# Optimization experiments

Measured on AMD Instinct MI355X. Metric: run time of the kernel, lower is better.

## Reference

```python
import jax, jax.numpy as jnp
import numpy as np
from jax import lax

B, T, C = 512, 128, 66
H, L, W = 512, 2, 10


def gru_cell(x, h, W_ih, W_hh, b_ih, b_hh):
    # PyTorch GRU gate order: r, z, n
    gi = x @ W_ih.T + b_ih            # [B, 3H]
    gh = h @ W_hh.T + b_hh            # [B, 3H]
    i_r, i_z, i_n = jnp.split(gi, 3, axis=-1)
    h_r, h_z, h_n = jnp.split(gh, 3, axis=-1)
    r = jax.nn.sigmoid(i_r + h_r)
    z = jax.nn.sigmoid(i_z + h_z)
    n = jnp.tanh(i_n + r * h_n)
    return (1.0 - z) * n + z * h


def setup_inputs() -> dict:
    key = jax.random.key(0)
    ks = jax.random.split(key, 16)
    s = 0.02
    inp = {
        "x": jax.random.normal(ks[0], (B, T, C), jnp.float32),
        # GRU layer 0 (input C -> hidden H)
        "W_ih0": jax.random.normal(ks[1], (3 * H, C), jnp.float32) * s,
        "W_hh0": jax.random.normal(ks[2], (3 * H, H), jnp.float32) * s,
        "b_ih0": jnp.zeros((3 * H,), jnp.float32),
        "b_hh0": jnp.zeros((3 * H,), jnp.float32),
        # GRU layer 1 (hidden H -> hidden H)
        "W_ih1": jax.random.normal(ks[3], (3 * H, H), jnp.float32) * s,
        "W_hh1": jax.random.normal(ks[4], (3 * H, H), jnp.float32) * s,
        "b_ih1": jnp.zeros((3 * H,), jnp.float32),
        "b_hh1": jnp.zeros((3 * H,), jnp.float32),
        # temporal_fc: Linear(window_size, 1) -> weight [1, W], bias [1]
        "temporal_w": jax.random.normal(ks[5], (1, W), jnp.float32) * s,
        "temporal_b": jnp.zeros((1,), jnp.float32),
        # spatial_fc: Linear(H, C)
        "spatial_w": jax.random.normal(ks[6], (C, H), jnp.float32) * s,
        "spatial_b": jnp.zeros((C,), jnp.float32),
    }
    return inp


def _forward(x, W_ih0, W_hh0, b_ih0, b_hh0, W_ih1, W_hh1, b_ih1, b_hh1,
             temporal_w, temporal_b, spatial_w, spatial_b):
    p0 = (W_ih0, W_hh0, b_ih0, b_hh0)
    p1 = (W_ih1, W_hh1, b_ih1, b_hh1)

    # ---- encoder: 2-layer GRU over the full sequence ----
    xs = jnp.transpose(x, (1, 0, 2))  # [T, B, C]
    h0 = jnp.zeros((x.shape[0], H), x.dtype)

    def make_step(p):
        def step(h, xt):
            hn = gru_cell(xt, h, *p)
            return hn, hn
        return step

    hT0, ys0 = lax.scan(make_step(p0), h0, xs)          # ys0 [T,B,H]
    hT1, ys1 = lax.scan(make_step(p1), h0, ys0)         # ys1 [T,B,H]

    encoder_window = jnp.transpose(ys1[-W:], (1, 0, 2))  # [B, W, H]
    last_input_frame = x[:, -1, :]                       # [B, C]

    def dec_step(carry, _):
        (h_0, h_1), win, dec_in = carry
        h_0n = gru_cell(dec_in, h_0, *p0)
        h_1n = gru_cell(h_0n, h_1, *p1)                  # decoder_out [B,H]
        win = jnp.concatenate([win[:, 1:, :], h_1n[:, None, :]], axis=1)
        # temporal_fc over window axis: [B,W,H] -> [B,H]
        t = jnp.einsum('bwh,w->bh', win, temporal_w[0]) + temporal_b[0]
        frame = t @ spatial_w.T + spatial_b + dec_in     # recursive residual
        return ((h_0n, h_1n), win, frame), frame

    init = ((hT0, hT1), encoder_window, last_input_frame)
    _, frames = lax.scan(dec_step, init, None, length=T)  # [T,B,C]
    return jnp.transpose(frames, (1, 0, 2))               # [B,T,C]


def reference(x, W_ih0, W_hh0, b_ih0, b_hh0, W_ih1, W_hh1, b_ih1, b_hh1,
              temporal_w, temporal_b, spatial_w, spatial_b):
    return _forward(x, W_ih0, W_hh0, b_ih0, b_hh0, W_ih1, W_hh1, b_ih1, b_hh1,
                    temporal_w, temporal_b, spatial_w, spatial_b)
```

## Files before the change

### kernel.cpp

```cpp
#include <hip/hip_runtime.h>
#include <hip/hip_bf16.h>

typedef __attribute__((ext_vector_type(8))) short bf16x8;
typedef __attribute__((ext_vector_type(4))) float f32x4;

#define NB 512
#define NT 128
#define NC 66
#define NH 512
#define NW 10
#define CP 96
#define BM 32
#define BJ 64
#define BK 32
#define BKP 40
#define NWG 256
#define NTHR 256
#define G3 1536

struct Params {
  const float *x, *Wih0, *Whh0, *bih0, *bhh0, *Wih1, *Whh1, *bih1, *bhh1, *tw, *tb, *sw, *sb;
  float *out;
  unsigned *barL, *barG;
  __hip_bfloat16 *Wih0h, *Wih0l;
  __hip_bfloat16 *Wch, *Wcl;
  float *cb;
  float *h0, *h1, *tvec;
  __hip_bfloat16 *winb;
};

__device__ __forceinline__ float sigmoidf_(float x) { return 1.f / (1.f + __expf(-x)); }
__device__ __forceinline__ float tanhf_(float x) {
  float e = __expf(2.f * x);
  return (e - 1.f) / (e + 1.f);
}
__device__ __forceinline__ void split2(float v, __hip_bfloat16& h, __hip_bfloat16& l) {
  h = __float2bfloat16(v);
  l = __float2bfloat16(v - __bfloat162float(h));
}
__device__ __forceinline__ unsigned short bfbits(__hip_bfloat16 h) { return *(unsigned short*)&h; }
__device__ __forceinline__ void splitpack4(float4 v, ushort4& ph, ushort4& pl) {
  __hip_bfloat16 h, l;
  split2(v.x, h, l); ph.x = bfbits(h); pl.x = bfbits(l);
  split2(v.y, h, l); ph.y = bfbits(h); pl.y = bfbits(l);
  split2(v.z, h, l); ph.z = bfbits(h); pl.z = bfbits(l);
  split2(v.w, h, l); ph.w = bfbits(h); pl.w = bfbits(l);
}

__device__ __forceinline__ float4 cload4(const float* p) {
  unsigned long long a = __hip_atomic_load((const unsigned long long*)p,       __ATOMIC_RELAXED, __HIP_MEMORY_SCOPE_AGENT);
  unsigned long long b = __hip_atomic_load(((const unsigned long long*)p) + 1, __ATOMIC_RELAXED, __HIP_MEMORY_SCOPE_AGENT);
  float4 r;
  ((unsigned long long*)&r)[0] = a;
  ((unsigned long long*)&r)[1] = b;
  return r;
}

__device__ __forceinline__ void gbar(unsigned* barL, unsigned* barG, unsigned& phase,
                                     int tid, int grp) {
  __syncthreads();
  ++phase;
  if (tid == 0) {
    unsigned old = __hip_atomic_fetch_add(&barL[grp * 32], 1u, __ATOMIC_RELEASE,
                                          __HIP_MEMORY_SCOPE_AGENT);
    if (old == phase * 32 - 1)
      __hip_atomic_fetch_add(barG, 1u, __ATOMIC_RELAXED, __HIP_MEMORY_SCOPE_AGENT);
    while (__hip_atomic_load(barG, __ATOMIC_RELAXED, __HIP_MEMORY_SCOPE_AGENT) < phase)
      __builtin_amdgcn_s_sleep(2);
  }
  __syncthreads();
  asm volatile("" ::: "memory");
}

#define AM_X 0
#define AM_H 2

__device__ __forceinline__ float4 loadA(int amode, const float* __restrict__ A, int tstep,
                                        int b0, int am, int k) {
  if (amode == AM_X) {
    const float* xr = A + ((size_t)(b0 + am) * NT + tstep) * NC;
    float4 v;
    v.x = (k + 0 < NC) ? xr[k + 0] : 0.f;
    v.y = (k + 1 < NC) ? xr[k + 1] : 0.f;
    v.z = (k + 2 < NC) ? xr[k + 2] : 0.f;
    v.w = (k + 3 < NC) ? xr[k + 3] : 0.f;
    return v;
  }
  return cload4(A + (size_t)(b0 + am) * NH + k);
}

__device__ __forceinline__ void zacc(f32x4 acc[2][4]) {
#pragma unroll
  for (int i = 0; i < 2; ++i)
#pragma unroll
    for (int g = 0; g < 4; ++g) {
      acc[i][g][0] = 0.f; acc[i][g][1] = 0.f; acc[i][g][2] = 0.f; acc[i][g][3] = 0.f;
    }
}

template <int G2, bool PSW>
__device__ __forceinline__ void gemm_tile(
    f32x4 acc[2][4],
    const __hip_bfloat16* __restrict__ Wh, const __hip_bfloat16* __restrict__ Wl,
    const float* __restrict__ Wf, int Kb,
    int amode, const float* __restrict__ A, int tstep,
    int b0, int j0,
    __hip_bfloat16* AsH, __hip_bfloat16* AsL,
    __hip_bfloat16* BsH, __hip_bfloat16* BsL,
    int tid)
{
  const int wv = tid >> 6, lane = tid & 63, quad = lane >> 4, l15 = lane & 15;
  const int ms = wv & 1, jh = wv >> 1;
  const int am = tid >> 3;
  const int ak = (tid & 7) << 2;
  const int nk = Kb >> 5;

  uint4 bh_[3], bl_[3];
  float4 w0_[3], w1_[3];

  auto fetchB = [&](int st) {
    const int kb = st << 5;
#pragma unroll
    for (int r = 0; r < 3; ++r) {
      const int l = tid + r * NTHR;
      const int nl = l >> 2, k8 = (l & 3) << 3;
      const int g = nl >> 6, jl = nl & 63;
      if (PSW) {
        const size_t o = (size_t)(g * NH + j0 + jl) * Kb + kb + k8;
        bh_[r] = *(const uint4*)(Wh + o);
        bl_[r] = *(const uint4*)(Wl + o);
      } else {
        const float* wp = Wf + (size_t)(g * NH + j0 + jl) * Kb + kb + k8;
        w0_[r] = *(const float4*)wp;
        w1_[r] = *(const float4*)(wp + 4);
      }
    }
  };

  float4 av = loadA(amode, A, tstep, b0, am, ak);
  fetchB(0);

  for (int st = 0; st < nk; ++st) {
    const int cur = st & 1;
    __hip_bfloat16* ah_d = AsH + cur * (BM * BKP);
    __hip_bfloat16* al_d = AsL + cur * (BM * BKP);
    __hip_bfloat16* bh_d = BsH + cur * (3 * BJ * BKP);
    __hip_bfloat16* bl_d = BsL + cur * (3 * BJ * BKP);
    {
      ushort4 ph, pl;
      splitpack4(av, ph, pl);
      *(ushort4*)(ah_d + am * BKP + ak) = ph;
      *(ushort4*)(al_d + am * BKP + ak) = pl;
    }
#pragma unroll
    for (int r = 0; r < 3; ++r) {
      const int l = tid + r * NTHR;
      const int nl = l >> 2, k8 = (l & 3) << 3;
      if (PSW) {
        *(uint4*)(bh_d + nl * BKP + k8) = bh_[r];
        *(uint4*)(bl_d + nl * BKP + k8) = bl_[r];
      } else {
        ushort4 ph0, pl0, ph1, pl1;
        splitpack4(w0_[r], ph0, pl0);
        splitpack4(w1_[r], ph1, pl1);
        *(ushort4*)(bh_d + nl * BKP + k8) = ph0;
        *(ushort4*)(bh_d + nl * BKP + k8 + 4) = ph1;
        *(ushort4*)(bl_d + nl * BKP + k8) = pl0;
        *(ushort4*)(bl_d + nl * BKP + k8 + 4) = pl1;
      }
    }
    if (st + 1 < nk) {
      av = loadA(amode, A, tstep, b0, am, ((st + 1) << 5) + ak);
      fetchB(st + 1);
    }
    __syncthreads();
    bf16x8 ah = *(const bf16x8*)(ah_d + (ms * 16 + l15) * BKP + quad * 8);
    bf16x8 al = *(const bf16x8*)(al_d + (ms * 16 + l15) * BKP + quad * 8);
#pragma unroll
    for (int jlf = 0; jlf < 2; ++jlf) {
      const int nbase = (jh * 32 + jlf * 16 + l15) * BKP + quad * 8;
      {
        bf16x8 bh = *(const bf16x8*)(bh_d + nbase);
        bf16x8 bl = *(const bf16x8*)(bl_d + nbase);
        acc[jlf][0] = __builtin_amdgcn_mfma_f32_16x16x32_bf16(ah, bh, acc[jlf][0], 0, 0, 0);
        acc[jlf][0] = __builtin_amdgcn_mfma_f32_16x16x32_bf16(al, bh, acc[jlf][0], 0, 0, 0);
        acc[jlf][0] = __builtin_amdgcn_mfma_f32_16x16x32_bf16(ah, bl, acc[jlf][0], 0, 0, 0);
      }
      {
        bf16x8 bh = *(const bf16x8*)(bh_d + BJ * BKP + nbase);
        bf16x8 bl = *(const bf16x8*)(bl_d + BJ * BKP + nbase);
        acc[jlf][1] = __builtin_amdgcn_mfma_f32_16x16x32_bf16(ah, bh, acc[jlf][1], 0, 0, 0);
        acc[jlf][1] = __builtin_amdgcn_mfma_f32_16x16x32_bf16(al, bh, acc[jlf][1], 0, 0, 0);
        acc[jlf][1] = __builtin_amdgcn_mfma_f32_16x16x32_bf16(ah, bl, acc[jlf][1], 0, 0, 0);
      }
      {
        bf16x8 bh = *(const bf16x8*)(bh_d + 2 * BJ * BKP + nbase);
        bf16x8 bl = *(const bf16x8*)(bl_d + 2 * BJ * BKP + nbase);
        acc[jlf][G2] = __builtin_amdgcn_mfma_f32_16x16x32_bf16(ah, bh, acc[jlf][G2], 0, 0, 0);
        acc[jlf][G2] = __builtin_amdgcn_mfma_f32_16x16x32_bf16(al, bh, acc[jlf][G2], 0, 0, 0);
        acc[jlf][G2] = __builtin_amdgcn_mfma_f32_16x16x32_bf16(ah, bl, acc[jlf][G2], 0, 0, 0);
      }
    }
  }
  __syncthreads();
}

__device__ __forceinline__ void ew_gru(
    f32x4 acc[2][4],
    const float* __restrict__ bi, const float* __restrict__ bh,
    const float* __restrict__ hold, float* __restrict__ hnew,
    int b0, int j0, int tid, __hip_bfloat16* win, int slot)
{
  const int wv = tid >> 6, lane = tid & 63, quad = lane >> 4, l15 = lane & 15;
  const int ms = wv & 1, jh = wv >> 1;
#pragma unroll
  for (int jlf = 0; jlf < 2; ++jlf) {
    const int j = j0 + jh * 32 + jlf * 16 + l15;
    const float br = bi[j] + bh[j];
    const float bz = bi[NH + j] + bh[NH + j];
    const float bni = bi[2 * NH + j];
    const float bnh = bh[2 * NH + j];
#pragma unroll
    for (int rg = 0; rg < 4; ++rg) {
      const int b = b0 + ms * 16 + quad * 4 + rg;
      const float r = sigmoidf_(acc[jlf][0][rg] + br);
      const float z = sigmoidf_(acc[jlf][1][rg] + bz);
      const float n = tanhf_(acc[jlf][2][rg] + bni + r * (acc[jlf][3][rg] + bnh));
      const float h = hold[(size_t)b * NH + j];
      const float hn = (1.f - z) * n + z * h;
      hnew[(size_t)b * NH + j] = hn;
      if (win) win[((size_t)b * NW + slot) * NH + j] = __float2bfloat16(hn);
    }
  }
}

__device__ __forceinline__ void ew_dec1(
    f32x4 acc[2][4], const Params& P, float* __restrict__ h1p,
    int b0, int j0, int tid, int s)
{
  const int wv = tid >> 6, lane = tid & 63, quad = lane >> 4, l15 = lane & 15;
  const int ms = wv & 1, jh = wv >> 1;
  const int slot = s % NW;
  float twv[NW];
#pragma unroll
  for (int k = 0; k < NW; ++k) {
    int idx = k - slot - 1; if (idx < 0) idx += NW;
    twv[k] = P.tw[idx];
  }
  const float tw9 = P.tw[NW - 1];
  const float tb0 = P.tb[0];
#pragma unroll
  for (int jlf = 0; jlf < 2; ++jlf) {
    const int j = j0 + jh * 32 + jlf * 16 + l15;
    const float br = P.bih1[j] + P.bhh1[j];
    const float bz = P.bih1[NH + j] + P.bhh1[NH + j];
    const float bni = P.bih1[2 * NH + j];
    const float bnh = P.bhh1[2 * NH + j];
#pragma unroll
    for (int rg = 0; rg < 4; ++rg) {
      const int b = b0 + ms * 16 + quad * 4 + rg;
      const float r = sigmoidf_(acc[jlf][0][rg] + br);
      const float z = sigmoidf_(acc[jlf][1][rg] + bz);
      const float n = tanhf_(acc[jlf][2][rg] + bni + r * (acc[jlf][3][rg] + bnh));
      const float h = h1p[(size_t)b * NH + j];
      const float hn = (1.f - z) * n + z * h;
      h1p[(size_t)b * NH + j] = hn;
      __hip_bfloat16* wrow = P.winb + (size_t)b * NW * NH + j;
      wrow[(size_t)slot * NH] = __float2bfloat16(hn);
      float ts = tb0 + hn * tw9;
#pragma unroll
      for (int k = 0; k < NW; ++k) {
        if (k == slot) continue;
        ts += __bfloat162float(wrow[(size_t)k * NH]) * twv[k];
      }
      P.tvec[(size_t)b * NH + j] = ts;
    }
  }
}

__global__ __launch_bounds__(NTHR) void rnn_kernel(Params P) {
  __shared__ __align__(16) __hip_bfloat16 AsH[2 * BM * BKP];
  __shared__ __align__(16) __hip_bfloat16 AsL[2 * BM * BKP];
  __shared__ __align__(16) __hip_bfloat16 BsH[2 * 3 * BJ * BKP];
  __shared__ __align__(16) __hip_bfloat16 BsL[2 * 3 * BJ * BKP];
  __shared__ __align__(16) float tl[4 * NH];
  const int tid = threadIdx.x;
  const int wg = blockIdx.x;
  const int grp = wg & 7;
  const size_t gid = (size_t)wg * NTHR + tid;
  const size_t GT = (size_t)NWG * NTHR;
  unsigned phase = 0;
  const int wv = tid >> 6, lane = tid & 63, l15 = lane & 15;
  const int jh = wv >> 1;

  for (size_t i = gid; i < (size_t)G3 * CP; i += GT) {
    const int row = (int)(i / CP), k = (int)(i - (size_t)row * CP);
    split2(k < NC ? P.Wih0[(size_t)row * NC + k] : 0.f, P.Wih0h[i], P.Wih0l[i]);
  }
  for (size_t i = gid; i < (size_t)G3 * NH; i += GT) {
    const int r = (int)(i >> 9), h = (int)(i & (NH - 1));
    float a = 0.f;
    for (int c = 0; c < NC; ++c) a += P.Wih0[(size_t)r * NC + c] * P.sw[(size_t)c * NH + h];
    split2(a, P.Wch[i], P.Wcl[i]);
  }
  for (size_t i = gid; i < (size_t)G3; i += GT) {
    float a = 0.f;
    for (int c = 0; c < NC; ++c) a += P.Wih0[i * NC + c] * P.sb[c];
    P.cb[i] = a;
  }
  for (size_t i = gid; i < (size_t)2 * NB * NH; i += GT) { P.h0[i] = 0.f; P.h1[i] = 0.f; }
  gbar(P.barL, P.barG, phase, tid, grp);

  const bool isL1 = wg >= 128;
  const int tile = wg & 127;
  const int b0 = (tile >> 3) * BM;
  const int j0 = (tile & 7) * BJ;

  float G[2][3][4];

  for (int t = 0; t <= NT; ++t) {
    const int cur = t & 1;
    float* h0c = P.h0 + (size_t)cur * NB * NH;
    float* h0n = P.h0 + (size_t)(cur ^ 1) * NB * NH;
    float* h1c = P.h1 + (size_t)cur * NB * NH;
    float* h1n = P.h1 + (size_t)(cur ^ 1) * NB * NH;
    f32x4 acc[2][4];
    if (!isL1) {
      if (t < NT) {
        zacc(acc);
        gemm_tile<2, true>(acc, P.Wih0h, P.Wih0l, nullptr, CP, AM_X, P.x, t, b0, j0, AsH, AsL, BsH, BsL, tid);
        gemm_tile<3, false>(acc, nullptr, nullptr, P.Whh0, NH, AM_H, h0c, 0, b0, j0, AsH, AsL, BsH, BsL, tid);
        ew_gru(acc, P.bih0, P.bhh0, h0c, h0n, b0, j0, tid, nullptr, 0);
      } else {
        zacc(acc);
        gemm_tile<2, true>(acc, P.Wih0h, P.Wih0l, nullptr, CP, AM_X, P.x, NT - 1, b0, j0, AsH, AsL, BsH, BsL, tid);
#pragma unroll
        for (int jlf = 0; jlf < 2; ++jlf)
#pragma unroll
          for (int c = 0; c < 3; ++c)
#pragma unroll
            for (int rg = 0; rg < 4; ++rg) G[jlf][c][rg] = acc[jlf][c][rg];
      }
    } else {
      if (t >= 1) {
        zacc(acc);
        gemm_tile<2, false>(acc, nullptr, nullptr, P.Wih1, NH, AM_H, h0c, 0, b0, j0, AsH, AsL, BsH, BsL, tid);
        gemm_tile<3, false>(acc, nullptr, nullptr, P.Whh1, NH, AM_H, h1c, 0, b0, j0, AsH, AsL, BsH, BsL, tid);
        ew_gru(acc, P.bih1, P.bhh1, h1c, h1n, b0, j0, tid,
               (t >= 119) ? P.winb : nullptr, t - 119);
      }
    }
    gbar(P.barL, P.barG, phase, tid, grp);
  }

  int d0 = 0;
  float* h1p = P.h1 + (size_t)NB * NH;

  float cbr[2][3];
  float Freg[2];
  if (!isL1) {
#pragma unroll
    for (int jlf = 0; jlf < 2; ++jlf)
#pragma unroll
      for (int c = 0; c < 3; ++c)
        cbr[jlf][c] = P.cb[c * NH + j0 + jh * 32 + jlf * 16 + l15];
#pragma unroll
    for (int v = 0; v < 2; ++v) {
      const int t2 = tid + v * NTHR;
      if (t2 < 4 * NC) {
        const int bl = t2 / NC, c = t2 - bl * NC, b = wg * 4 + bl;
        Freg[v] = P.x[((size_t)b * NT + (NT - 1)) * NC + c];
      }
    }
  }

  auto frame_out = [&](int sout) {
    const float* tvb = P.tvec + (size_t)wg * 4 * NH;
    *(float4*)&tl[tid * 8] = cload4(tvb + tid * 8);
    *(float4*)&tl[tid * 8 + 4] = cload4(tvb + tid * 8 + 4);
    __syncthreads();
#pragma unroll
    for (int v = 0; v < 2; ++v) {
      const int t2 = tid + v * NTHR;
      if (t2 < 4 * NC) {
        const int bl = t2 / NC, c = t2 - bl * NC, b = wg * 4 + bl;
        float f = Freg[v] + P.sb[c];
        const float4* swr = (const float4*)(P.sw + (size_t)c * NH);
        const float4* tr = (const float4*)(tl + bl * NH);
#pragma unroll 8
        for (int h4 = 0; h4 < NH / 4; ++h4) {
          float4 tv = tr[h4], wv4 = swr[h4];
          f += tv.x * wv4.x + tv.y * wv4.y + tv.z * wv4.z + tv.w * wv4.w;
        }
        Freg[v] = f;
        P.out[((size_t)b * NT + sout) * NC + c] = f;
      }
    }
    __syncthreads();
  };

  for (int s = 0; s < NT; ++s) {
    float* h0c = P.h0 + (size_t)d0 * NB * NH;
    float* h0n = P.h0 + (size_t)(d0 ^ 1) * NB * NH;
    f32x4 acc[2][4];
    if (!isL1) {
      if (s >= 1) frame_out(s - 1);
      zacc(acc);
      if (s >= 1)
        gemm_tile<2, true>(acc, P.Wch, P.Wcl, nullptr, NH, AM_H, P.tvec, 0, b0, j0, AsH, AsL, BsH, BsL, tid);
#pragma unroll
      for (int jlf = 0; jlf < 2; ++jlf)
#pragma unroll
        for (int c = 0; c < 3; ++c)
#pragma unroll
          for (int rg = 0; rg < 4; ++rg) {
            float g = G[jlf][c][rg] + acc[jlf][c][rg] + (s >= 1 ? cbr[jlf][c] : 0.f);
            G[jlf][c][rg] = g;
            acc[jlf][c][rg] = g;
          }
      gemm_tile<3, false>(acc, nullptr, nullptr, P.Whh0, NH, AM_H, h0c, 0, b0, j0, AsH, AsL, BsH, BsL, tid);
      ew_gru(acc, P.bih0, P.bhh0, h0c, h0n, b0, j0, tid, nullptr, 0);
    } else {
      zacc(acc);
      gemm_tile<3, false>(acc, nullptr, nullptr, P.Whh1, NH, AM_H, h1p, 0, b0, j0, AsH, AsL, BsH, BsL, tid);
    }
    gbar(P.barL, P.barG, phase, tid, grp);
    if (isL1) {
      gemm_tile<2, false>(acc, nullptr, nullptr, P.Wih1, NH, AM_H, h0n, 0, b0, j0, AsH, AsL, BsH, BsL, tid);
      ew_dec1(acc, P, h1p, b0, j0, tid, s);
    }
    gbar(P.barL, P.barG, phase, tid, grp);
    d0 ^= 1;
  }
  if (!isL1) frame_out(NT - 1);
}

extern "C" void kernel_launch(void* const* d_in, const int* in_sizes, int n_in,
                              void* d_out, int out_size, void* d_ws, size_t ws_size,
                              hipStream_t stream) {
  (void)in_sizes; (void)n_in; (void)out_size; (void)ws_size;
  Params P;
  P.x    = (const float*)d_in[0];
  P.Wih0 = (const float*)d_in[1];
  P.Whh0 = (const float*)d_in[2];
  P.bih0 = (const float*)d_in[3];
  P.bhh0 = (const float*)d_in[4];
  P.Wih1 = (const float*)d_in[5];
  P.Whh1 = (const float*)d_in[6];
  P.bih1 = (const float*)d_in[7];
  P.bhh1 = (const float*)d_in[8];
  P.tw   = (const float*)d_in[9];
  P.tb   = (const float*)d_in[10];
  P.sw   = (const float*)d_in[11];
  P.sb   = (const float*)d_in[12];
  P.out  = (float*)d_out;

  char* w = (char*)d_ws;
  size_t used = 0;
  auto take = [&](size_t bytes) {
    char* p = w + used;
    used += (bytes + 255) & ~(size_t)255;
    return p;
  };
  unsigned* bar = (unsigned*)take(2048);
  P.barL = bar;
  P.barG = bar + 8 * 32;
  P.Wih0h = (__hip_bfloat16*)take((size_t)G3 * CP * 2);
  P.Wih0l = (__hip_bfloat16*)take((size_t)G3 * CP * 2);
  P.Wch   = (__hip_bfloat16*)take((size_t)G3 * NH * 2);
  P.Wcl   = (__hip_bfloat16*)take((size_t)G3 * NH * 2);
  P.cb    = (float*)take((size_t)G3 * 4);
  P.h0    = (float*)take((size_t)2 * NB * NH * 4);
  P.h1    = (float*)take((size_t)2 * NB * NH * 4);
  P.tvec  = (float*)take((size_t)NB * NH * 4);
  P.winb  = (__hip_bfloat16*)take((size_t)NB * NW * NH * 2);

  hipMemsetAsync(d_ws, 0, 2048, stream);
  rnn_kernel<<<dim3(NWG), dim3(NTHR), 0, stream>>>(P);
}
```

Before: 15.82 ms.

## Remap workgroups by XCD and pre-split recurrent weights into bf16 hi/lo

Each workgroup reads its XCC_ID and gets a rank ordered by XCD, so tiles that share weight columns (j0) land on the same XCD and its L2. The barrier target is scaled by 8 to count per-XCD groups. When the workspace is large enough, the recurrent weights Whh0, Wih1 and Whh1 are split into bf16 hi/lo once at startup, so each step no longer converts fp32 weights. The cost is extra workspace, extra startup work, and an assumption that XCD counts line up with the 8 barrier groups.

```diff
diff --git a/kernel.cpp b/kernel.cpp
--- a/kernel.cpp
+++ b/kernel.cpp
@@ -22,11 +22,13 @@
   const float *x, *Wih0, *Whh0, *bih0, *bhh0, *Wih1, *Whh1, *bih1, *bhh1, *tw, *tb, *sw, *sb;
   float *out;
   unsigned *barL, *barG;
+  int *xcnt, *xrank;
   __hip_bfloat16 *Wih0h, *Wih0l;
   __hip_bfloat16 *Wch, *Wcl;
   float *cb;
   float *h0, *h1, *tvec;
   __hip_bfloat16 *winb;
+  __hip_bfloat16 *Whh0h, *Whh0l, *Wih1h, *Wih1l, *Whh1h, *Whh1l;
 };
 
 __device__ __forceinline__ float sigmoidf_(float x) { return 1.f / (1.f + __expf(-x)); }
@@ -58,6 +60,7 @@
 
 __device__ __forceinline__ void gbar(unsigned* barL, unsigned* barG, unsigned& phase,
                                      int tid, int grp) {
+  asm volatile("s_waitcnt vmcnt(0)" ::: "memory");
   __syncthreads();
   ++phase;
   if (tid == 0) {
@@ -65,7 +68,7 @@
                                           __HIP_MEMORY_SCOPE_AGENT);
     if (old == phase * 32 - 1)
       __hip_atomic_fetch_add(barG, 1u, __ATOMIC_RELAXED, __HIP_MEMORY_SCOPE_AGENT);
-    while (__hip_atomic_load(barG, __ATOMIC_RELAXED, __HIP_MEMORY_SCOPE_AGENT) < phase)
+    while (__hip_atomic_load(barG, __ATOMIC_RELAXED, __HIP_MEMORY_SCOPE_AGENT) < phase * 8u)
       __builtin_amdgcn_s_sleep(2);
   }
   __syncthreads();
@@ -106,8 +109,7 @@
     int amode, const float* __restrict__ A, int tstep,
     int b0, int j0,
     __hip_bfloat16* AsH, __hip_bfloat16* AsL,
-    __hip_bfloat16* BsH, __hip_bfloat16* BsL,
-    int tid)
+    __hip_bfloat16* BsH, __hip_bfloat16* BsL, int tid)
 {
   const int wv = tid >> 6, lane = tid & 63, quad = lane >> 4, l15 = lane & 15;
   const int ms = wv & 1, jh = wv >> 1;
@@ -278,12 +280,15 @@
   }
 }
 
+template <bool PS>
 __global__ __launch_bounds__(NTHR) void rnn_kernel(Params P) {
   __shared__ __align__(16) __hip_bfloat16 AsH[2 * BM * BKP];
   __shared__ __align__(16) __hip_bfloat16 AsL[2 * BM * BKP];
   __shared__ __align__(16) __hip_bfloat16 BsH[2 * 3 * BJ * BKP];
   __shared__ __align__(16) __hip_bfloat16 BsL[2 * 3 * BJ * BKP];
   __shared__ __align__(16) float tl[4 * NH];
+  __shared__ int sxcd;
+  __shared__ int sgi;
   const int tid = threadIdx.x;
   const int wg = blockIdx.x;
   const int grp = wg & 7;
@@ -293,6 +298,14 @@
   const int wv = tid >> 6, lane = tid & 63, l15 = lane & 15;
   const int jh = wv >> 1;
 
+  if (tid == 0) {
+    unsigned x;
+    asm volatile("s_getreg_b32 %0, hwreg(HW_REG_XCC_ID)" : "=s"(x));
+    x &= 7;
+    sxcd = (int)x;
+    __hip_atomic_fetch_add(&P.xcnt[x * 32], 1, __ATOMIC_RELAXED, __HIP_MEMORY_SCOPE_AGENT);
+  }
+
   for (size_t i = gid; i < (size_t)G3 * CP; i += GT) {
     const int row = (int)(i / CP), k = (int)(i - (size_t)row * CP);
     split2(k < NC ? P.Wih0[(size_t)row * NC + k] : 0.f, P.Wih0h[i], P.Wih0l[i]);
@@ -303,6 +316,13 @@
     for (int c = 0; c < NC; ++c) a += P.Wih0[(size_t)r * NC + c] * P.sw[(size_t)c * NH + h];
     split2(a, P.Wch[i], P.Wcl[i]);
   }
+  if (PS) {
+    for (size_t i = gid; i < (size_t)G3 * NH; i += GT) {
+      split2(P.Whh0[i], P.Whh0h[i], P.Whh0l[i]);
+      split2(P.Wih1[i], P.Wih1h[i], P.Wih1l[i]);
+      split2(P.Whh1[i], P.Whh1h[i], P.Whh1l[i]);
+    }
+  }
   for (size_t i = gid; i < (size_t)G3; i += GT) {
     float a = 0.f;
     for (int c = 0; c < NC; ++c) a += P.Wih0[i * NC + c] * P.sb[c];
@@ -311,10 +331,22 @@
   for (size_t i = gid; i < (size_t)2 * NB * NH; i += GT) { P.h0[i] = 0.f; P.h1[i] = 0.f; }
   gbar(P.barL, P.barG, phase, tid, grp);
 
-  const bool isL1 = wg >= 128;
-  const int tile = wg & 127;
-  const int b0 = (tile >> 3) * BM;
-  const int j0 = (tile & 7) * BJ;
+  if (tid == 0) {
+    const int myx = sxcd;
+    int pre = 0;
+    for (int e = 0; e < myx; ++e)
+      pre += __hip_atomic_load(&P.xcnt[e * 32], __ATOMIC_RELAXED, __HIP_MEMORY_SCOPE_AGENT);
+    int rank = __hip_atomic_fetch_add(&P.xrank[myx * 32], 1, __ATOMIC_RELAXED,
+                                      __HIP_MEMORY_SCOPE_AGENT);
+    sgi = pre + rank;
+  }
+  __syncthreads();
+  const int gi = sgi;
+  const bool isL1 = gi >= 128;
+  const int local = gi & 127;
+  const int q = local >> 5, r5 = local & 31;
+  const int j0 = (2 * q + (r5 >> 4)) * BJ;
+  const int b0 = (r5 & 15) * BM;
 
   float G[2][3][4];
 
@@ -329,7 +361,7 @@
       if (t < NT) {
         zacc(acc);
         gemm_tile<2, true>(acc, P.Wih0h, P.Wih0l, nullptr, CP, AM_X, P.x, t, b0, j0, AsH, AsL, BsH, BsL, tid);
-        gemm_tile<3, false>(acc, nullptr, nullptr, P.Whh0, NH, AM_H, h0c, 0, b0, j0, AsH, AsL, BsH, BsL, tid);
+        gemm_tile<3, PS>(acc, P.Whh0h, P.Whh0l, P.Whh0, NH, AM_H, h0c, 0, b0, j0, AsH, AsL, BsH, BsL, tid);
         ew_gru(acc, P.bih0, P.bhh0, h0c, h0n, b0, j0, tid, nullptr, 0);
       } else {
         zacc(acc);
@@ -344,8 +376,8 @@
     } else {
       if (t >= 1) {
         zacc(acc);
-        gemm_tile<2, false>(acc, nullptr, nullptr, P.Wih1, NH, AM_H, h0c, 0, b0, j0, AsH, AsL, BsH, BsL, tid);
-        gemm_tile<3, false>(acc, nullptr, nullptr, P.Whh1, NH, AM_H, h1c, 0, b0, j0, AsH, AsL, BsH, BsL, tid);
+        gemm_tile<2, PS>(acc, P.Wih1h, P.Wih1l, P.Wih1, NH, AM_H, h0c, 0, b0, j0, AsH, AsL, BsH, BsL, tid);
+        gemm_tile<3, PS>(acc, P.Whh1h, P.Whh1l, P.Whh1, NH, AM_H, h1c, 0, b0, j0, AsH, AsL, BsH, BsL, tid);
         ew_gru(acc, P.bih1, P.bhh1, h1c, h1n, b0, j0, tid,
                (t >= 119) ? P.winb : nullptr, t - 119);
       }
@@ -368,14 +400,14 @@
     for (int v = 0; v < 2; ++v) {
       const int t2 = tid + v * NTHR;
       if (t2 < 4 * NC) {
-        const int bl = t2 / NC, c = t2 - bl * NC, b = wg * 4 + bl;
+        const int bl = t2 / NC, c = t2 - bl * NC, b = gi * 4 + bl;
         Freg[v] = P.x[((size_t)b * NT + (NT - 1)) * NC + c];
       }
     }
   }
 
   auto frame_out = [&](int sout) {
-    const float* tvb = P.tvec + (size_t)wg * 4 * NH;
+    const float* tvb = P.tvec + (size_t)gi * 4 * NH;
     *(float4*)&tl[tid * 8] = cload4(tvb + tid * 8);
     *(float4*)&tl[tid * 8 + 4] = cload4(tvb + tid * 8 + 4);
     __syncthreads();
@@ -383,7 +415,7 @@
     for (int v = 0; v < 2; ++v) {
       const int t2 = tid + v * NTHR;
       if (t2 < 4 * NC) {
-        const int bl = t2 / NC, c = t2 - bl * NC, b = wg * 4 + bl;
+        const int bl = t2 / NC, c = t2 - bl * NC, b = gi * 4 + bl;
         float f = Freg[v] + P.sb[c];
         const float4* swr = (const float4*)(P.sw + (size_t)c * NH);
         const float4* tr = (const float4*)(tl + bl * NH);
@@ -418,15 +450,15 @@
             G[jlf][c][rg] = g;
             acc[jlf][c][rg] = g;
           }
-      gemm_tile<3, false>(acc, nullptr, nullptr, P.Whh0, NH, AM_H, h0c, 0, b0, j0, AsH, AsL, BsH, BsL, tid);
+      gemm_tile<3, PS>(acc, P.Whh0h, P.Whh0l, P.Whh0, NH, AM_H, h0c, 0, b0, j0, AsH, AsL, BsH, BsL, tid);
       ew_gru(acc, P.bih0, P.bhh0, h0c, h0n, b0, j0, tid, nullptr, 0);
     } else {
       zacc(acc);
-      gemm_tile<3, false>(acc, nullptr, nullptr, P.Whh1, NH, AM_H, h1p, 0, b0, j0, AsH, AsL, BsH, BsL, tid);
+      gemm_tile<3, PS>(acc, P.Whh1h, P.Whh1l, P.Whh1, NH, AM_H, h1p, 0, b0, j0, AsH, AsL, BsH, BsL, tid);
     }
     gbar(P.barL, P.barG, phase, tid, grp);
     if (isL1) {
-      gemm_tile<2, false>(acc, nullptr, nullptr, P.Wih1, NH, AM_H, h0n, 0, b0, j0, AsH, AsL, BsH, BsL, tid);
+      gemm_tile<2, PS>(acc, P.Wih1h, P.Wih1l, P.Wih1, NH, AM_H, h0n, 0, b0, j0, AsH, AsL, BsH, BsL, tid);
       ew_dec1(acc, P, h1p, b0, j0, tid, s);
     }
     gbar(P.barL, P.barG, phase, tid, grp);
@@ -438,7 +470,7 @@
 extern "C" void kernel_launch(void* const* d_in, const int* in_sizes, int n_in,
                               void* d_out, int out_size, void* d_ws, size_t ws_size,
                               hipStream_t stream) {
-  (void)in_sizes; (void)n_in; (void)out_size; (void)ws_size;
+  (void)in_sizes; (void)n_in; (void)out_size;
   Params P;
   P.x    = (const float*)d_in[0];
   P.Wih0 = (const float*)d_in[1];
@@ -463,8 +495,10 @@
     return p;
   };
   unsigned* bar = (unsigned*)take(2048);
-  P.barL = bar;
-  P.barG = bar + 8 * 32;
+  P.barL  = bar;
+  P.barG  = bar + 8 * 32;
+  P.xcnt  = (int*)take(1024);
+  P.xrank = (int*)take(1024);
   P.Wih0h = (__hip_bfloat16*)take((size_t)G3 * CP * 2);
   P.Wih0l = (__hip_bfloat16*)take((size_t)G3 * CP * 2);
   P.Wch   = (__hip_bfloat16*)take((size_t)G3 * NH * 2);
@@ -474,7 +508,19 @@
   P.h1    = (float*)take((size_t)2 * NB * NH * 4);
   P.tvec  = (float*)take((size_t)NB * NH * 4);
   P.winb  = (__hip_bfloat16*)take((size_t)NB * NW * NH * 2);
-
-  hipMemsetAsync(d_ws, 0, 2048, stream);
-  rnn_kernel<<<dim3(NWG), dim3(NTHR), 0, stream>>>(P);
-}
+  size_t big = ((size_t)G3 * NH * 2 + 255) & ~(size_t)255;
+  char* opt = w + used;
+  bool presplit = ws_size >= used + 6 * big;
+  P.Whh0h = (__hip_bfloat16*)(opt + 0 * big);
+  P.Whh0l = (__hip_bfloat16*)(opt + 1 * big);
+  P.Wih1h = (__hip_bfloat16*)(opt + 2 * big);
+  P.Wih1l = (__hip_bfloat16*)(opt + 3 * big);
+  P.Whh1h = (__hip_bfloat16*)(opt + 4 * big);
+  P.Whh1l = (__hip_bfloat16*)(opt + 5 * big);
+
+  hipMemsetAsync(d_ws, 0, 4096, stream);
+  if (presplit)
+    rnn_kernel<true><<<dim3(NWG), dim3(NTHR), 0, stream>>>(P);
+  else
+    rnn_kernel<false><<<dim3(NWG), dim3(NTHR), 0, stream>>>(P);
+}
```

Measured after the change: 34.47 ms. 118% more time.
